# Kernel tuning notes

Measured on AMD Instinct MI355X. Metric: run time of the kernel, lower is better.

## Reference

```python
import jax, jax.numpy as jnp
import numpy as np
from jax import lax

BINS = 256
HSIG = 0.01
MS_WEIGHTS = np.array([0.0448, 0.2856, 0.3001, 0.2363, 0.1333], dtype=np.float32)


def _conv(x, w, b=None, pad='SAME', groups=1):
    out = lax.conv_general_dilated(x, w, (1, 1), pad,
                                   feature_group_count=groups,
                                   dimension_numbers=('NCHW', 'OIHW', 'NCHW'))
    if b is not None:
        out = out + b[None, :, None, None]
    return out


def _avg_pool(x, k):
    B, C, H, W = x.shape
    return x.reshape(B, C, H // k, k, W // k, k).mean(axis=(3, 5))


def _max_pool2(x):
    return lax.reduce_window(x, -jnp.inf, lax.max, (1, 1, 2, 2), (1, 1, 2, 2), 'VALID')


def _gauss_win():
    c = jnp.arange(11, dtype=jnp.float32) - 5.0
    g = jnp.exp(-(c * c) / (2.0 * 1.5 * 1.5))
    return g / g.sum()


def _gauss_filter(x, win):
    C = x.shape[1]
    wh = jnp.tile(win.reshape(1, 1, 11, 1), (C, 1, 1, 1))
    ww = jnp.tile(win.reshape(1, 1, 1, 11), (C, 1, 1, 1))
    x = _conv(x, wh, pad='VALID', groups=C)
    return _conv(x, ww, pad='VALID', groups=C)


def _ssim(X, Y, win):
    C1, C2 = 0.01 ** 2, 0.03 ** 2
    mu1 = _gauss_filter(X, win)
    mu2 = _gauss_filter(Y, win)
    s11 = _gauss_filter(X * X, win) - mu1 * mu1
    s22 = _gauss_filter(Y * Y, win) - mu2 * mu2
    s12 = _gauss_filter(X * Y, win) - mu1 * mu2
    cs = (2.0 * s12 + C2) / (s11 + s22 + C2)
    ssim = ((2.0 * mu1 * mu2 + C1) / (mu1 * mu1 + mu2 * mu2 + C1)) * cs
    return ssim.mean(axis=(2, 3)), cs.mean(axis=(2, 3))  # (B,C) each


def _ms_ssim(X, Y):
    win = _gauss_win()
    vals = []
    for i in range(5):
        s, c = _ssim(X, Y, win)
        vals.append(jax.nn.relu(s if i == 4 else c))
        if i < 4:
            X = _avg_pool(X, 2)
            Y = _avg_pool(Y, 2)
    v = jnp.stack(vals)  # (5,B,C)
    w = jnp.asarray(MS_WEIGHTS)[:, None, None]
    return jnp.prod(v ** w, axis=0).mean()


def _soft_hist(y, edges):
    # faithful to source: broadcast every pixel against 256 Gaussian bins,
    # sum over dim 0 (batch), then normalize to a distribution.
    h = jnp.exp(-0.5 * ((y[..., None] - edges) / HSIG) ** 2).sum(axis=0)  # (C,H,W,BINS)
    return h / h.sum()


def _vgg_feats(x, ws, bs):
    # VGG19 features[:16]: conv1_1..conv3_3, maxpool after conv idx 1 and 3.
    for i, (w, b) in enumerate(zip(ws, bs)):
        x = jax.nn.relu(_conv(x, w, b))
        if i in (1, 3):
            x = _max_pool2(x)
    return x


def combined_loss(y_true, y_pred, ws, bs):
    B, C, H, W = y_pred.shape
    diff = y_pred - y_true
    ad = jnp.abs(diff)
    # smooth L1 (beta=1)
    l1 = jnp.mean(jnp.where(ad < 1.0, 0.5 * diff * diff, ad - 0.5))
    # MS-SSIM loss
    msssim_l = 1.0 - _ms_ssim(y_true, y_pred)
    # VGG perceptual
    f1 = _vgg_feats(y_true, ws, bs)
    f2 = _vgg_feats(y_pred, ws, bs)
    perc = jnp.mean((f1 - f2) ** 2)
    # soft histogram
    edges = jnp.linspace(0.0, 1.0, BINS, dtype=jnp.float32)
    hist_l = jnp.mean(jnp.abs(_soft_hist(y_true, edges) - _soft_hist(y_pred, edges)))
    # PSNR loss: 40 - (-10*log10(mse))
    mse = jnp.mean(diff * diff)
    psnr_l = 40.0 + 10.0 * jnp.log10(mse)
    # color loss
    color_l = jnp.mean(jnp.abs(y_true.mean(axis=(1, 2, 3)) - y_pred.mean(axis=(1, 2, 3))))
    # exposure loss (16x16 avg pool of channel mean, target 0.6)
    exp_l = jnp.mean((_avg_pool(y_pred.mean(axis=1, keepdims=True), 16) - 0.6) ** 2)
    # illumination smoothness (counts faithful to source)
    hv = jnp.sum((y_pred[:, :, 1:, :] - y_pred[:, :, :-1, :]) ** 2)
    wv = jnp.sum((y_pred[:, :, :, 1:] - y_pred[:, :, :, :-1]) ** 2)
    ill = 2.0 * (hv / ((W - 1) * C) + wv / (W * (C - 1))) / B
    # spatial consistency: 4 neighbor-difference kernels on 4x4-pooled luminance
    K = jnp.array([[[0, 0, 0], [-1, 1, 0], [0, 0, 0]],
                   [[0, 0, 0], [0, 1, -1], [0, 0, 0]],
                   [[0, -1, 0], [0, 1, 0], [0, 0, 0]],
                   [[0, 0, 0], [0, 1, 0], [0, -1, 0]]], dtype=jnp.float32)[:, None]  # (4,1,3,3)
    op = _avg_pool(y_true.mean(axis=1, keepdims=True), 4)
    ep = _avg_pool(y_pred.mean(axis=1, keepdims=True), 4)
    spat = jnp.sum((_conv(op, K) - _conv(ep, K)) ** 2, axis=1, keepdims=True)  # (B,1,H/4,W/4)
    total = (1.0 * l1 + 0.06 * perc + 0.05 * hist_l + 0.0083 * psnr_l
             + 0.25 * color_l + 0.5 * msssim_l + 0.1 * exp_l + 0.1 * ill + 0.1 * spat)
    return jnp.mean(total)


def setup_inputs() -> dict:
    key = jax.random.key(0)
    ks = jax.random.split(key, 16)
    B, H, W = 2, 224, 224
    y_true = jax.random.uniform(ks[0], (B, 3, H, W), dtype=jnp.float32)
    y_pred = jax.random.uniform(ks[1], (B, 3, H, W), dtype=jnp.float32)
    chans = [(64, 3), (64, 64), (128, 64), (128, 128), (256, 128), (256, 256), (256, 256)]
    inp = {'y_true': y_true, 'y_pred': y_pred}
    for i, (co, ci) in enumerate(chans):
        std = float(np.sqrt(2.0 / (ci * 9)))
        inp[f'w{i}'] = jax.random.normal(ks[2 + i], (co, ci, 3, 3), dtype=jnp.float32) * std
        inp[f'b{i}'] = jnp.zeros((co,), dtype=jnp.float32)
    return inp


def reference(y_true, y_pred, w0, w1, w2, w3, w4, w5, w6, b0, b1, b2, b3, b4, b5, b6):
    ws = [w0, w1, w2, w3, w4, w5, w6]
    bs = [b0, b1, b2, b3, b4, b5, b6]
    return combined_loss(y_true, y_pred, ws, bs)
```

## Files before the change

kernel.cpp:

```cpp
#include <hip/hip_runtime.h>
#include <cmath>

typedef __attribute__((ext_vector_type(8))) short  short8;
typedef __attribute__((ext_vector_type(4))) float  floatx4;
typedef __attribute__((ext_vector_type(8))) unsigned short ushort8;
typedef __attribute__((ext_vector_type(8))) unsigned char uchar8v;

#define SLOT(i) ((i) * 16)
#define ACC_L1   0
#define ACC_MSE  1
#define ACC_ST0  2
#define ACC_ST1  3
#define ACC_SP0  4
#define ACC_SP1  5
#define ACC_HV   6
#define ACC_WV   7
#define ACC_EXP  8
#define ACC_SPAT 9
#define ACC_PERC 10
#define SSIM_SLOT(scale, cs, img) (256 + ((scale) * 12 + (cs) * 6 + (img)) * 16)

struct GW { float g[11]; };

__device__ __forceinline__ float waveSum(float v) {
#pragma unroll
  for (int o = 32; o > 0; o >>= 1) v += __shfl_down(v, o, 64);
  return v;
}

__device__ __forceinline__ float blockSum256(float v) {
  __shared__ float red[4];
  const int tid = threadIdx.x;
  v = waveSum(v);
  __syncthreads();
  if ((tid & 63) == 0) red[tid >> 6] = v;
  __syncthreads();
  return red[0] + red[1] + red[2] + red[3];
}

__device__ __forceinline__ unsigned int pk_fp8x4(float v0, float v1, float v2, float v3) {
  int p = __builtin_amdgcn_cvt_pk_fp8_f32(v0, v1, 0, false);
  p = __builtin_amdgcn_cvt_pk_fp8_f32(v2, v3, p, true);
  return (unsigned int)p;
}


struct PrepArgs {
  const float* w[6];
  int co[6], ci[6];
  int wcum[7];
  unsigned char* zp[6];
  int zH[6], zC[6];
  int zcum[7];
};

struct MegaArgs {
  PrepArgs pa;
  unsigned char* wdst;
  const float* w0;
  const float* b0;
  unsigned char* c1;
  float* pyrX;
  float* pyrY;
  float* acc;
  int nPrep, nBasic, nPyr, nPS;
};

__global__ __launch_bounds__(256) void mega_k(MegaArgs A,
                                              const float* __restrict__ yt,
                                              const float* __restrict__ yp) {
  __shared__ float smem[684];
  const int tid = threadIdx.x;
  int bid = blockIdx.x;

  if (bid < A.nPrep) {
    const int idx = bid * 256 + tid;
    const PrepArgs& a = A.pa;
    if (idx < a.wcum[6]) {
      int L = 0;
      while (idx >= a.wcum[L + 1]) ++L;
      const int r = idx - a.wcum[L];
      const int Cin = a.ci[L];
      const int cin = r % Cin;
      const int t = r / Cin;
      const int tap = t % 9;
      const int cout = t / 9;
      const float v = a.w[L][((size_t)cout * Cin + cin) * 9 + tap] * 8.0f;
      A.wdst[idx] = (unsigned char)(__builtin_amdgcn_cvt_pk_fp8_f32(v, v, 0, false) & 0xff);
      return;
    }
    const int zi = idx - a.wcum[6];
    if (zi >= a.zcum[6]) return;
    int b = 0;
    while (zi >= a.zcum[b + 1]) ++b;
    const int H = a.zH[b], C = a.zC[b];
    const int rowE = (H + 2) * C;
    const int per = 2 * rowE + 2 * H * C;
    int k = zi - a.zcum[b];
    const int pl = k / per;
    const int k0 = k - pl * per;
    size_t o;
    if (k0 < rowE) o = k0;
    else if (k0 < 2 * rowE) o = (size_t)(H + 1) * rowE + (k0 - rowE);
    else {
      const int kk = k0 - 2 * rowE;
      const int y = kk / (2 * C) + 1;
      const int r = kk % (2 * C);
      const int x = (r < C) ? 0 : (H + 1);
      const int c = (r < C) ? r : (r - C);
      o = (size_t)y * rowE + (size_t)x * C + c;
    }
    a.zp[b][(size_t)pl * (H + 2) * rowE + o] = 0;
    return;
  }
  bid -= A.nPrep;

  if (bid < A.nBasic) {
    float* acc = A.acc;
    const int i4 = bid * 256 + tid;
    const int idx = i4 * 4;
    const float4 t4 = *(const float4*)(yt + idx);
    const float4 p4 = *(const float4*)(yp + idx);
    float l1 = 0.f, mse = 0.f, st0 = 0.f, st1 = 0.f, sp0 = 0.f, sp1 = 0.f, hv = 0.f, wv = 0.f;
#define BTERM(tt, pp) { const float d = (pp) - (tt); const float ad = fabsf(d); \
                        l1 += (ad < 1.f) ? 0.5f * d * d : ad - 0.5f; mse += d * d; }
    BTERM(t4.x, p4.x) BTERM(t4.y, p4.y) BTERM(t4.z, p4.z) BTERM(t4.w, p4.w)
#undef BTERM
    const float ts = t4.x + t4.y + t4.z + t4.w;
    const float ps = p4.x + p4.y + p4.z + p4.w;
    if (i4 < 37632) { st0 = ts; sp0 = ps; } else { st1 = ts; sp1 = ps; }
    const int h = (idx / 224) % 224;
    if (h < 223) {
      const float4 pn = *(const float4*)(yp + idx + 224);
      float d;
      d = pn.x - p4.x; hv += d * d;
      d = pn.y - p4.y; hv += d * d;
      d = pn.z - p4.z; hv += d * d;
      d = pn.w - p4.w; hv += d * d;
    }
    {
      const int w = idx % 224;
      float d;
      d = p4.y - p4.x; wv += d * d;
      d = p4.z - p4.y; wv += d * d;
      d = p4.w - p4.z; wv += d * d;
      if (w < 220) { d = yp[idx + 4] - p4.w; wv += d * d; }
    }
    float s;
    s = blockSum256(l1);  if (tid == 0) atomicAdd(acc + SLOT(ACC_L1), s);
    s = blockSum256(mse); if (tid == 0) atomicAdd(acc + SLOT(ACC_MSE), s);
    s = blockSum256(st0); if (tid == 0) atomicAdd(acc + SLOT(ACC_ST0), s);
    s = blockSum256(st1); if (tid == 0) atomicAdd(acc + SLOT(ACC_ST1), s);
    s = blockSum256(sp0); if (tid == 0) atomicAdd(acc + SLOT(ACC_SP0), s);
    s = blockSum256(sp1); if (tid == 0) atomicAdd(acc + SLOT(ACC_SP1), s);
    s = blockSum256(hv);  if (tid == 0) atomicAdd(acc + SLOT(ACC_HV), s);
    s = blockSum256(wv);  if (tid == 0) atomicAdd(acc + SLOT(ACC_WV), s);
    return;
  }
  bid -= A.nBasic;

  if (bid < A.nPyr) {
    float (*sA)[17] = (float(*)[17])smem;
    float (*s1)[9]  = (float(*)[9])(smem + 272);
    float (*s2)[5]  = (float(*)[5])(smem + 344);
    float (*s3)[3]  = (float(*)[3])(smem + 364);
    const int tile = bid % 196;
    const int img = (bid / 196) % 6;
    const int zt = bid / (196 * 6);
    const int ty = tile / 14, tx = tile - ty * 14;
    const float* src = (zt ? yp : yt) + (size_t)img * 224 * 224;
    float* dst = zt ? A.pyrY : A.pyrX;
    const int r = tid >> 4, c = tid & 15;
    sA[r][c] = src[(size_t)(ty * 16 + r) * 224 + tx * 16 + c];
    __syncthreads();
    if (tid < 64) {
      const int r1 = tid >> 3, c1 = tid & 7;
      const float m = 0.25f * (sA[2 * r1][2 * c1] + sA[2 * r1][2 * c1 + 1] +
                               sA[2 * r1 + 1][2 * c1] + sA[2 * r1 + 1][2 * c1 + 1]);
      dst[(size_t)img * 12544 + (ty * 8 + r1) * 112 + tx * 8 + c1] = m;
      s1[r1][c1] = m;
    }
    __syncthreads();
    if (tid < 16) {
      const int r2 = tid >> 2, c2 = tid & 3;
      const float m = 0.25f * (s1[2 * r2][2 * c2] + s1[2 * r2][2 * c2 + 1] +
                               s1[2 * r2 + 1][2 * c2] + s1[2 * r2 + 1][2 * c2 + 1]);
      dst[75264 + (size_t)img * 3136 + (ty * 4 + r2) * 56 + tx * 4 + c2] = m;
      s2[r2][c2] = m;
    }
    __syncthreads();
    if (tid < 4) {
      const int r3 = tid >> 1, c3 = tid & 1;
      const float m = 0.25f * (s2[2 * r3][2 * c3] + s2[2 * r3][2 * c3 + 1] +
                               s2[2 * r3 + 1][2 * c3] + s2[2 * r3 + 1][2 * c3 + 1]);
      dst[94080 + (size_t)img * 784 + (ty * 2 + r3) * 28 + tx * 2 + c3] = m;
      s3[r3][c3] = m;
    }
    __syncthreads();
    if (tid == 0) {
      const float m = 0.25f * (s3[0][0] + s3[0][1] + s3[1][0] + s3[1][1]);
      dst[98784 + (size_t)img * 196 + ty * 14 + tx] = m;
    }
    return;
  }
  bid -= A.nPyr;

  if (bid < A.nPS) {
    float* acc = A.acc;
    float (*sOp)[19] = (float(*)[19])smem;
    float (*sEp)[19] = (float(*)[19])(smem + 342);
    const int b = bid >> 4;
    const int tq = bid & 15;
    const int ty0 = (tq >> 2) * 16, tx0 = (tq & 3) * 16;
    for (int e = tid; e < 18 * 18; e += 256) {
      const int r = e / 18, c = e - (e / 18) * 18;
      const int gy = ty0 - 1 + r, gx = tx0 - 1 + c;
      float vo = 0.f, ve = 0.f;
      if (gy >= 0 && gy < 56 && gx >= 0 && gx < 56) {
        float so = 0.f, se = 0.f;
        for (int ch = 0; ch < 3; ++ch)
#pragma unroll
          for (int dy = 0; dy < 4; ++dy) {
            const size_t off = (((size_t)b * 3 + ch) * 224 + (gy * 4 + dy)) * 224 + gx * 4;
            const float4 a = *(const float4*)(yt + off);
            const float4 ee = *(const float4*)(yp + off);
            so += a.x + a.y + a.z + a.w;
            se += ee.x + ee.y + ee.z + ee.w;
          }
        vo = so * (1.f / 48.f);
        ve = se * (1.f / 48.f);
      }
      sOp[r][c] = vo; sEp[r][c] = ve;
    }
    __syncthreads();
    float v = 0.f;
    {
      const int r = tid >> 4, c = tid & 15;
      const int gy = ty0 + r, gx = tx0 + c;
      if (gy < 56 && gx < 56) {
        const float oc = sOp[r + 1][c + 1], ec = sEp[r + 1][c + 1];
        const float ol = sOp[r + 1][c],     el = sEp[r + 1][c];
        const float orr = sOp[r + 1][c + 2], er = sEp[r + 1][c + 2];
        const float ou = sOp[r][c + 1],     eu = sEp[r][c + 1];
        const float od = sOp[r + 2][c + 1], ed = sEp[r + 2][c + 1];
        float d;
        d = (oc - ol) - (ec - el);   v += d * d;
        d = (oc - orr) - (ec - er);  v += d * d;
        d = (oc - ou) - (ec - eu);   v += d * d;
        d = (oc - od) - (ec - ed);   v += d * d;
      }
    }
    const float t = blockSum256(v);
    if (tid == 0) atomicAdd(acc + SLOT(ACC_SPAT), t);
    if (tid < 16) {
      const int ey = tid >> 2, ex = tid & 3;
      if (ty0 + 4 * ey < 56 && tx0 + 4 * ex < 56) {
        float ssum = 0.f;
#pragma unroll
        for (int dy = 0; dy < 4; ++dy)
#pragma unroll
          for (int dx = 0; dx < 4; ++dx)
            ssum += sEp[4 * ey + dy + 1][4 * ex + dx + 1];
        const float m = ssum * (1.f / 16.f) - 0.6f;
        atomicAdd(acc + SLOT(ACC_EXP), m * m);
      }
    }
    return;
  }
  bid -= A.nPS;

  {
    float (*sIn)[10][12] = (float(*)[10][12])smem;
    const int zf = bid / 784;
    const int rem = bid - zf * 784;
    const int by = rem / 28, bx = rem - by * 28;
    const int tx = tid & 7, ty = (tid >> 3) & 7, tz = tid >> 6;
    const int img = zf >> 1;
    const int zb = zf & 1;
    const float* in = ((img >> 1) ? yp : yt) + (size_t)(img & 1) * 3 * 224 * 224;
    const int x0 = bx << 3, y0 = by << 3;
    const int x = x0 + tx, y = y0 + ty;
    int wrow = (zb * 32 + tz * 8) * 27;
    wrow = __builtin_amdgcn_readfirstlane(wrow);

    for (int el = tid; el < 300; el += 256) {
      const int ci = el / 100;
      const int r2 = el - ci * 100;
      const int r = r2 / 10, cl = r2 - r * 10;
      const int gy = y0 - 1 + r, gx = x0 - 1 + cl;
      float v = 0.f;
      if (gy >= 0 && gy < 224 && gx >= 0 && gx < 224)
        v = in[((size_t)ci * 224 + gy) * 224 + gx];
      sIn[ci][r][cl] = v;
    }
    __syncthreads();

    float a[8];
#pragma unroll
    for (int j = 0; j < 8; ++j) a[j] = 0.f;
#pragma unroll
    for (int ci = 0; ci < 3; ++ci) {
      float xv[9];
#pragma unroll
      for (int ky = 0; ky < 3; ++ky)
#pragma unroll
        for (int kx = 0; kx < 3; ++kx)
          xv[ky * 3 + kx] = sIn[ci][ty + ky][tx + kx];
      const float* wp = A.w0 + wrow + ci * 9;
#pragma unroll
      for (int j = 0; j < 8; ++j)
#pragma unroll
        for (int k = 0; k < 9; ++k)
          a[j] = fmaf(xv[k], wp[27 * j + k], a[j]);
    }
    const int coB = zb * 32 + tz * 8;
    float r[8];
#pragma unroll
    for (int j = 0; j < 8; ++j) r[j] = fmaxf(a[j] + A.b0[coB + j], 0.f);
    const size_t o = (((size_t)(zb * 4 + img) * 226 + (y + 1)) * 226 + (x + 1)) * 32 + tz * 8;
    uint2 rv;
    rv.x = pk_fp8x4(r[0], r[1], r[2], r[3]);
    rv.y = pk_fp8x4(r[4], r[5], r[6], r[7]);
    *(uint2*)(A.c1 + o) = rv;
  }
}

__global__ __launch_bounds__(256) void ssim_all_k(const float* __restrict__ yt,
                                                  const float* __restrict__ yp,
                                                  const float* __restrict__ pyrX,
                                                  const float* __restrict__ pyrY,
                                                  float* __restrict__ acc, GW gw) {
  __shared__ float sX[26][27], sY[26][27];
  __shared__ float sV[5][16][27];
  const int bid = blockIdx.x;
  int s = 0;
  if (bid >= 196) s = 1;
  if (bid >= 245) s = 2;
  if (bid >= 254) s = 3;
  if (bid >= 258) s = 4;
  const int cumA[5]   = {0, 196, 245, 254, 258};
  const int tilesA[5] = {14, 7, 3, 2, 1};
  const int dimsA[5]  = {224, 112, 56, 28, 14};
  const int offsA[5]  = {0, 0, 75264, 94080, 98784};
  const int t = bid - cumA[s];
  const int tiles = tilesA[s];
  const int n = dimsA[s];
  const int m = n - 10;
  const int tid = threadIdx.x;
  const int img = blockIdx.y;
  const int ty0 = (t / tiles) * 16;
  const int tx0 = (t - (t / tiles) * tiles) * 16;
  const float* Xb = ((s == 0) ? yt : pyrX + offsA[s]) + (size_t)img * n * n;
  const float* Yb = ((s == 0) ? yp : pyrY + offsA[s]) + (size_t)img * n * n;

  for (int e = tid; e < 26 * 26; e += 256) {
    const int r = e / 26, c = e - (e / 26) * 26;
    const int gy = ty0 + r, gx = tx0 + c;
    float xv = 0.f, yv = 0.f;
    if (gy < n && gx < n) {
      xv = Xb[(size_t)gy * n + gx];
      yv = Yb[(size_t)gy * n + gx];
    }
    sX[r][c] = xv; sY[r][c] = yv;
  }
  __syncthreads();

  for (int e = tid; e < 16 * 26; e += 256) {
    const int r = e / 26, c = e - (e / 26) * 26;
    float sx = 0.f, sy = 0.f, sxx = 0.f, syy = 0.f, sxy = 0.f;
#pragma unroll
    for (int tt = 0; tt < 11; ++tt) {
      const float xv = sX[r + tt][c];
      const float yv = sY[r + tt][c];
      const float g = gw.g[tt];
      sx += g * xv; sy += g * yv;
      sxx += g * xv * xv; syy += g * yv * yv; sxy += g * xv * yv;
    }
    sV[0][r][c] = sx; sV[1][r][c] = sy;
    sV[2][r][c] = sxx; sV[3][r][c] = syy; sV[4][r][c] = sxy;
  }
  __syncthreads();

  float sv = 0.f, cv = 0.f;
  {
    const int r = tid >> 4, c = tid & 15;
    if (ty0 + r < m && tx0 + c < m) {
      float mu1 = 0.f, mu2 = 0.f, e11 = 0.f, e22 = 0.f, e12 = 0.f;
#pragma unroll
      for (int tt = 0; tt < 11; ++tt) {
        const float g = gw.g[tt];
        mu1 += g * sV[0][r][c + tt];
        mu2 += g * sV[1][r][c + tt];
        e11 += g * sV[2][r][c + tt];
        e22 += g * sV[3][r][c + tt];
        e12 += g * sV[4][r][c + tt];
      }
      const float C1 = 1e-4f, C2 = 9e-4f;
      const float s11 = e11 - mu1 * mu1;
      const float s22 = e22 - mu2 * mu2;
      const float s12 = e12 - mu1 * mu2;
      cv = (2.f * s12 + C2) / (s11 + s22 + C2);
      sv = ((2.f * mu1 * mu2 + C1) / (mu1 * mu1 + mu2 * mu2 + C1)) * cv;
    }
  }
  float tsum = blockSum256(sv);
  if (tid == 0) atomicAdd(acc + SSIM_SLOT(s, 0, img), tsum);
  tsum = blockSum256(cv);
  if (tid == 0) atomicAdd(acc + SSIM_SLOT(s, 1, img), tsum);
}

template<int CIN>
__global__ __launch_bounds__(256, 4) void conv_mfma(
    const unsigned char* __restrict__ in, const unsigned char* __restrict__ wtp,
    const float* __restrict__ bias, unsigned char* __restrict__ out,
    int W, int rowsPI) {
  constexpr int NSLAB = CIN / 32;
  constexpr int ASTB = 304;
  constexpr int BSTB = 48;
  constexpr int NBRUN = 6 * 66;
  constexpr int NACH = 32 * 18;
  constexpr int NBCH = NBRUN * 2;
  __shared__ unsigned char As[32 * ASTB];
  __shared__ unsigned char Bs[NBRUN * BSTB];

  const int tid = threadIdx.x;
  const int lane = tid & 63;
  const int wave = tid >> 6;
  const int quad = lane >> 4;
  const int lr = lane & 15;
  const int img = blockIdx.y / rowsPI;
  const int y0 = (blockIdx.y - img * rowsPI) * 4;
  const int x0 = blockIdx.x * 64;
  const int cob = blockIdx.z * 32;
  const int Wp = W + 2;
  const int H = rowsPI * 4;
  const size_t IPL = (size_t)(H + 2) * Wp * 32;
  const unsigned char* inI = in + (size_t)img * IPL;
  unsigned char* outI = out + ((size_t)blockIdx.z * 4 + img) * IPL;

  floatx4 acc[2][4];
#pragma unroll
  for (int m = 0; m < 2; ++m)
#pragma unroll
    for (int n = 0; n < 4; ++n) acc[m][n] = (floatx4){0.f, 0.f, 0.f, 0.f};

  const int abase = lr * ASTB + quad * 8;

  for (int s = 0; s < NSLAB; ++s) {
    __syncthreads();
#pragma unroll
    for (int i = 0; i < (NACH + 255) / 256; ++i) {
      const int ee = tid + i * 256;
      if (ee < NACH) {
        const int cout = ee / 18;
        const int rem = ee - cout * 18;
        const int tap = rem >> 1;
        const int part = rem & 1;
        const uint4 v = *(const uint4*)(wtp + ((size_t)(cob + cout) * 9 + tap) * CIN + s * 32 + part * 16);
        *(uint4*)(As + cout * ASTB + tap * 32 + part * 16) = v;
      }
    }
#pragma unroll
    for (int i = 0; i < (NBCH + 255) / 256; ++i) {
      const int ee = tid + i * 256;
      if (ee < NBCH) {
        const int part = ee & 1;
        const int run = ee >> 1;
        const int row = run / 66;
        const int px = run - row * 66;
        uint4 v = {0, 0, 0, 0};
        const int gx = x0 + px;
        if (gx < Wp)
          v = *(const uint4*)(inI + (size_t)s * 4 * IPL +
                              ((size_t)(y0 + row) * Wp + gx) * 32 + part * 16);
        *(uint4*)(Bs + run * BSTB + part * 16) = v;
      }
    }
    __syncthreads();

#pragma unroll
    for (int dy = 0; dy < 3; ++dy)
#pragma unroll
      for (int dx = 0; dx < 3; ++dx) {
        const int tap = dy * 3 + dx;
        const long af0 = *(const long*)(As + abase + tap * 32);
        const long af1 = *(const long*)(As + abase + 16 * ASTB + tap * 32);
        long bfr[4];
#pragma unroll
        for (int n = 0; n < 4; ++n)
          bfr[n] = *(const long*)(Bs + ((wave + dy) * 66 + n * 16 + lr + dx) * BSTB + quad * 8);
#pragma unroll
        for (int n = 0; n < 4; ++n) {
          acc[0][n] = __builtin_amdgcn_mfma_f32_16x16x32_fp8_fp8(af0, bfr[n], acc[0][n], 0, 0, 0);
          acc[1][n] = __builtin_amdgcn_mfma_f32_16x16x32_fp8_fp8(af1, bfr[n], acc[1][n], 0, 0, 0);
        }
      }
  }

#pragma unroll
  for (int m = 0; m < 2; ++m) {
    const int cb = cob + m * 16 + quad * 4;
#pragma unroll
    for (int n = 0; n < 4; ++n) {
      const int px = x0 + n * 16 + lr;
      if (px < W) {
        const float v0 = fmaxf(acc[m][n].x * 0.125f + bias[cb + 0], 0.f);
        const float v1 = fmaxf(acc[m][n].y * 0.125f + bias[cb + 1], 0.f);
        const float v2 = fmaxf(acc[m][n].z * 0.125f + bias[cb + 2], 0.f);
        const float v3 = fmaxf(acc[m][n].w * 0.125f + bias[cb + 3], 0.f);
        *(unsigned int*)(outI + ((size_t)(y0 + wave + 1) * Wp + px + 1) * 32 +
                         m * 16 + quad * 4) = pk_fp8x4(v0, v1, v2, v3);
      }
    }
  }
}

__global__ __launch_bounds__(256) void pool_nhwc(const unsigned char* __restrict__ in,
                                                 unsigned char* __restrict__ out,
                                                 int Ho, int Wo, int C) {
  const int per = Ho * Wo * (C / 8);
  const int idx = blockIdx.x * 256 + threadIdx.x;
  if (idx >= 4 * per) return;
  const int img = idx / per;
  const int k = idx - img * per;
  const int c8 = k % (C / 8);
  const int p = k / (C / 8);
  const int x = p % Wo, y = p / Wo;
  const int zb = c8 >> 2;
  const int cw = (c8 & 3) * 8;
  const int Wi = 2 * Wo + 2;
  const unsigned char* ib = in + ((size_t)(zb * 4 + img) * (2 * Ho + 2) * Wi +
                                  (size_t)(2 * y + 1) * Wi + (2 * x + 1)) * 32 + cw;
  const uchar8v a = *(const uchar8v*)(ib);
  const uchar8v b = *(const uchar8v*)(ib + 32);
  const uchar8v d = *(const uchar8v*)(ib + (size_t)Wi * 32);
  const uchar8v e = *(const uchar8v*)(ib + (size_t)Wi * 32 + 32);
  const uchar8v r = __builtin_elementwise_max(__builtin_elementwise_max(a, b),
                                              __builtin_elementwise_max(d, e));
  *(uchar8v*)(out + ((size_t)(zb * 4 + img) * (Ho + 2) * (Wo + 2) +
                     (size_t)(y + 1) * (Wo + 2) + (x + 1)) * 32 + cw) = r;
}

#define FP8D(av, bv, J) { const float dd = __builtin_amdgcn_cvt_f32_fp8((av), (J)) - \
                                           __builtin_amdgcn_cvt_f32_fp8((bv), (J)); \
                          v = fmaf(dd, dd, v); }
__global__ __launch_bounds__(256) void perc_k(const unsigned char* __restrict__ f,
                                              float* __restrict__ acc) {
  const int PER = 56 * 56 * 256 / 8;
  const size_t PL = (size_t)58 * 58 * 32;
  float v = 0.f;
  for (int ch = blockIdx.x * 256 + threadIdx.x; ch < 2 * PER; ch += 256 * 256) {
    const int q = ch / PER;
    const int r = ch - q * PER;
    const int e = r * 8;
    const int c = e & 255;
    const int p = e >> 8;
    const int x = p % 56, y = p / 56;
    const int zb = c >> 5;
    const int cw = c & 31;
    const size_t o = (size_t)(zb * 4 + q) * PL + ((size_t)(y + 1) * 58 + (x + 1)) * 32 + cw;
    const uint2 a = *(const uint2*)(f + o);
    const uint2 b = *(const uint2*)(f + o + 2 * PL);
    FP8D(a.x, b.x, 0) FP8D(a.x, b.x, 1) FP8D(a.x, b.x, 2) FP8D(a.x, b.x, 3)
    FP8D(a.y, b.y, 0) FP8D(a.y, b.y, 1) FP8D(a.y, b.y, 2) FP8D(a.y, b.y, 3)
  }
  const float t = blockSum256(v);
  if (threadIdx.x == 0) atomicAdd(acc + SLOT(ACC_PERC), t);
}

__global__ void final_k(const float* __restrict__ acc, float* __restrict__ out) {
  if (threadIdx.x != 0 || blockIdx.x != 0) return;
  const float NPIX = 2.f * 3.f * 224.f * 224.f;
  const float l1 = acc[SLOT(ACC_L1)] / NPIX;
  const float mse = acc[SLOT(ACC_MSE)] / NPIX;
  const float psnr = 40.f + 10.f * log10f(mse);
  const float cm = 1.f / (3.f * 224.f * 224.f);
  const float color = 0.5f * (fabsf(acc[SLOT(ACC_ST0)] - acc[SLOT(ACC_SP0)]) +
                              fabsf(acc[SLOT(ACC_ST1)] - acc[SLOT(ACC_SP1)])) * cm;
  const float ill = acc[SLOT(ACC_HV)] / 669.f + acc[SLOT(ACC_WV)] / 448.f;
  const float expl = acc[SLOT(ACC_EXP)] / 392.f;
  const float spat = acc[SLOT(ACC_SPAT)] / 6272.f;
  const float perc = acc[SLOT(ACC_PERC)] / 1605632.f;
  const float wms[5] = {0.0448f, 0.2856f, 0.3001f, 0.2363f, 0.1333f};
  const int ns[5] = {214, 102, 46, 18, 4};
  float msum = 0.f;
  for (int img = 0; img < 6; ++img) {
    float prod = 1.f;
    for (int s = 0; s < 5; ++s) {
      const float denom = (float)(ns[s] * ns[s]);
      float v = (s == 4) ? acc[SSIM_SLOT(s, 0, img)] / denom
                         : acc[SSIM_SLOT(s, 1, img)] / denom;
      v = fmaxf(v, 0.f);
      prod *= powf(v, wms[s]);
    }
    msum += prod;
  }
  const float msssim = msum / 6.f;
  out[0] = l1 + 0.06f * perc + 0.0083f * psnr + 0.25f * color +
           0.5f * (1.f - msssim) + 0.1f * expl + 0.1f * ill + 0.1f * spat;
}

extern "C" void kernel_launch(void* const* d_in, const int* in_sizes, int n_in,
                              void* d_out, int out_size, void* d_ws, size_t ws_size,
                              hipStream_t stream) {
  const float* yt = (const float*)d_in[0];
  const float* yp = (const float*)d_in[1];
  const float* W7[7]; const float* B7[7];
  for (int i = 0; i < 7; ++i) {
    W7[i] = (const float*)d_in[2 + 2 * i];
    B7[i] = (const float*)d_in[3 + 2 * i];
  }

  char* ws = (char*)d_ws;
  float* acc = (float*)ws;
  size_t off = 16384;
  auto align256 = [&]() { off = (off + 255) & ~(size_t)255; };
  align256(); unsigned char* C1  = (unsigned char*)(ws + off); off += (size_t)4 * 226 * 226 * 64;
  align256(); unsigned char* T0  = (unsigned char*)(ws + off); off += (size_t)4 * 226 * 226 * 64;
  align256(); unsigned char* Pl1 = (unsigned char*)(ws + off); off += (size_t)4 * 114 * 114 * 64;
  align256(); unsigned char* C3  = (unsigned char*)(ws + off); off += (size_t)4 * 114 * 114 * 128;
  align256(); unsigned char* Pl2 = (unsigned char*)(ws + off); off += (size_t)4 * 58 * 58 * 128;
  align256(); unsigned char* C5  = (unsigned char*)(ws + off); off += (size_t)4 * 58 * 58 * 256;
  align256(); unsigned char* C6  = (unsigned char*)(ws + off); off += (size_t)4 * 58 * 58 * 256;
  align256(); unsigned char* F   = (unsigned char*)(ws + off); off += (size_t)4 * 58 * 58 * 256;
  align256(); unsigned char* WT  = (unsigned char*)(ws + off); off += (size_t)1732608;
  align256(); float* pyrX = (float*)(ws + off); off += (size_t)100000 * 4;
  align256(); float* pyrY = (float*)(ws + off); off += (size_t)100000 * 4;
  if (ws_size < off) return;

  GW gw;
  {
    double vv[11]; double s = 0.0;
    for (int i = 0; i < 11; ++i) { const double c = i - 5.0; vv[i] = exp(-(c * c) / 4.5); s += vv[i]; }
    for (int i = 0; i < 11; ++i) gw.g[i] = (float)(vv[i] / s);
  }

  hipMemsetAsync(acc, 0, 16384, stream);

  const int co[7] = {64, 64, 128, 128, 256, 256, 256};
  const int ci[7] = {3, 64, 64, 128, 128, 256, 256};
  MegaArgs ma;
  size_t wtOff[7];
  {
    int e = 0;
    for (int i = 1; i < 7; ++i) {
      ma.pa.w[i - 1] = W7[i]; ma.pa.co[i - 1] = co[i]; ma.pa.ci[i - 1] = ci[i];
      ma.pa.wcum[i - 1] = e; wtOff[i] = (size_t)e; e += co[i] * 9 * ci[i];
    }
    ma.pa.wcum[6] = e;
    unsigned char* bufs[6] = {C1, Pl1, C3, Pl2, C5, C6};
    const int hh[6] = {224, 112, 112, 56, 56, 56};
    const int cc[6] = {64, 64, 128, 128, 256, 256};
    int z = 0;
    for (int i = 0; i < 6; ++i) {
      ma.pa.zp[i] = bufs[i]; ma.pa.zH[i] = hh[i]; ma.pa.zC[i] = 32;
      ma.pa.zcum[i] = z;
      z += (4 * cc[i] / 32) * (2 * (hh[i] + 2) * 32 + 2 * hh[i] * 32);
    }
    ma.pa.zcum[6] = z;
    ma.nPrep = (ma.pa.wcum[6] + z + 255) / 256;
  }
  ma.wdst = WT;
  ma.w0 = W7[0]; ma.b0 = B7[0];
  ma.c1 = C1;
  ma.pyrX = pyrX; ma.pyrY = pyrY;
  ma.acc = acc;
  ma.nBasic = 294;
  ma.nPyr = 196 * 6 * 2;
  ma.nPS = 32;
  const int nConv1 = 28 * 28 * 8;
  const int megaBlocks = ma.nPrep + ma.nBasic + ma.nPyr + ma.nPS + nConv1;

  mega_k<<<megaBlocks, 256, 0, stream>>>(ma, yt, yp);
  ssim_all_k<<<dim3(259, 6), 256, 0, stream>>>(yt, yp, pyrX, pyrY, acc, gw);

  conv_mfma<64> <<<dim3(4, 4 * 56, 2), 256, 0, stream>>>(C1,  WT + wtOff[1], B7[1], T0, 224, 56);
  pool_nhwc<<<(4 * 112 * 112 * 8 + 255) / 256, 256, 0, stream>>>(T0, Pl1, 112, 112, 64);
  conv_mfma<64> <<<dim3(2, 4 * 28, 4), 256, 0, stream>>>(Pl1, WT + wtOff[2], B7[2], C3, 112, 28);
  conv_mfma<128><<<dim3(2, 4 * 28, 4), 256, 0, stream>>>(C3,  WT + wtOff[3], B7[3], T0, 112, 28);
  pool_nhwc<<<(4 * 56 * 56 * 16 + 255) / 256, 256, 0, stream>>>(T0, Pl2, 56, 56, 128);
  conv_mfma<128><<<dim3(1, 4 * 14, 8), 256, 0, stream>>>(Pl2, WT + wtOff[4], B7[4], C5, 56, 14);
  conv_mfma<256><<<dim3(1, 4 * 14, 8), 256, 0, stream>>>(C5,  WT + wtOff[5], B7[5], C6, 56, 14);
  conv_mfma<256><<<dim3(1, 4 * 14, 8), 256, 0, stream>>>(C6,  WT + wtOff[6], B7[6], F,  56, 14);
  perc_k<<<256, 256, 0, stream>>>(F, acc);

  final_k<<<1, 64, 0, stream>>>(acc, (float*)d_out);
}
```

Before: 301.8 us.

## Move full-res SSIM into mega kernel, reorder blocks, vectorize weight prep and padding

Moves the scale-0 SSIM tiles, which read only the raw inputs, out of the separate SSIM kernel and into the mega kernel. The slower SSIM and conv1 blocks are scheduled first, and the follow-up kernel now handles only the pyramid scales. Weight fp8 conversion now writes 4 bytes per thread and border zeroing writes 16 bytes per thread, which cuts the number of prep blocks. The cost is larger shared memory per block in the mega kernel, which may lower occupancy for every branch.

```diff
diff --git a/kernel.cpp b/kernel.cpp
--- a/kernel.cpp
+++ b/kernel.cpp
@@ -50,7 +50,7 @@
   int co[6], ci[6];
   int wcum[7];
   unsigned char* zp[6];
-  int zH[6], zC[6];
+  int zH[6];
   int zcum[7];
 };
 
@@ -63,57 +63,187 @@
   float* pyrX;
   float* pyrY;
   float* acc;
-  int nPrep, nBasic, nPyr, nPS;
+  GW gw;
+  int nSsim0, nConv1, nPyr, nBasic, nPS, nPrep, nW4;
 };
 
 __global__ __launch_bounds__(256) void mega_k(MegaArgs A,
                                               const float* __restrict__ yt,
                                               const float* __restrict__ yp) {
-  __shared__ float smem[684];
+  __shared__ float smem[3564];
   const int tid = threadIdx.x;
   int bid = blockIdx.x;
 
-  if (bid < A.nPrep) {
-    const int idx = bid * 256 + tid;
-    const PrepArgs& a = A.pa;
-    if (idx < a.wcum[6]) {
-      int L = 0;
-      while (idx >= a.wcum[L + 1]) ++L;
-      const int r = idx - a.wcum[L];
-      const int Cin = a.ci[L];
-      const int cin = r % Cin;
-      const int t = r / Cin;
-      const int tap = t % 9;
-      const int cout = t / 9;
-      const float v = a.w[L][((size_t)cout * Cin + cin) * 9 + tap] * 8.0f;
-      A.wdst[idx] = (unsigned char)(__builtin_amdgcn_cvt_pk_fp8_f32(v, v, 0, false) & 0xff);
-      return;
-    }
-    const int zi = idx - a.wcum[6];
-    if (zi >= a.zcum[6]) return;
-    int b = 0;
-    while (zi >= a.zcum[b + 1]) ++b;
-    const int H = a.zH[b], C = a.zC[b];
-    const int rowE = (H + 2) * C;
-    const int per = 2 * rowE + 2 * H * C;
-    int k = zi - a.zcum[b];
-    const int pl = k / per;
-    const int k0 = k - pl * per;
-    size_t o;
-    if (k0 < rowE) o = k0;
-    else if (k0 < 2 * rowE) o = (size_t)(H + 1) * rowE + (k0 - rowE);
-    else {
-      const int kk = k0 - 2 * rowE;
-      const int y = kk / (2 * C) + 1;
-      const int r = kk % (2 * C);
-      const int x = (r < C) ? 0 : (H + 1);
-      const int c = (r < C) ? r : (r - C);
-      o = (size_t)y * rowE + (size_t)x * C + c;
-    }
-    a.zp[b][(size_t)pl * (H + 2) * rowE + o] = 0;
+  if (bid < A.nSsim0) {
+    float* acc = A.acc;
+    float (*sX)[27] = (float(*)[27])smem;
+    float (*sY)[27] = (float(*)[27])(smem + 702);
+    float (*sV)[16][27] = (float(*)[16][27])(smem + 1404);
+    const int img = bid / 196;
+    const int t = bid - img * 196;
+    const int n = 224, m = 214;
+    const int ty0 = (t / 14) * 16;
+    const int tx0 = (t - (t / 14) * 14) * 16;
+    const float* Xb = yt + (size_t)img * n * n;
+    const float* Yb = yp + (size_t)img * n * n;
+    for (int e = tid; e < 26 * 26; e += 256) {
+      const int r = e / 26, c = e - (e / 26) * 26;
+      const int gy = ty0 + r, gx = tx0 + c;
+      float xv = 0.f, yv = 0.f;
+      if (gy < n && gx < n) {
+        xv = Xb[(size_t)gy * n + gx];
+        yv = Yb[(size_t)gy * n + gx];
+      }
+      sX[r][c] = xv; sY[r][c] = yv;
+    }
+    __syncthreads();
+    for (int e = tid; e < 16 * 26; e += 256) {
+      const int r = e / 26, c = e - (e / 26) * 26;
+      float sx = 0.f, sy = 0.f, sxx = 0.f, syy = 0.f, sxy = 0.f;
+#pragma unroll
+      for (int tt = 0; tt < 11; ++tt) {
+        const float xv = sX[r + tt][c];
+        const float yv = sY[r + tt][c];
+        const float g = A.gw.g[tt];
+        sx += g * xv; sy += g * yv;
+        sxx += g * xv * xv; syy += g * yv * yv; sxy += g * xv * yv;
+      }
+      sV[0][r][c] = sx; sV[1][r][c] = sy;
+      sV[2][r][c] = sxx; sV[3][r][c] = syy; sV[4][r][c] = sxy;
+    }
+    __syncthreads();
+    float sv = 0.f, cv = 0.f;
+    {
+      const int r = tid >> 4, c = tid & 15;
+      if (ty0 + r < m && tx0 + c < m) {
+        float mu1 = 0.f, mu2 = 0.f, e11 = 0.f, e22 = 0.f, e12 = 0.f;
+#pragma unroll
+        for (int tt = 0; tt < 11; ++tt) {
+          const float g = A.gw.g[tt];
+          mu1 += g * sV[0][r][c + tt];
+          mu2 += g * sV[1][r][c + tt];
+          e11 += g * sV[2][r][c + tt];
+          e22 += g * sV[3][r][c + tt];
+          e12 += g * sV[4][r][c + tt];
+        }
+        const float C1 = 1e-4f, C2 = 9e-4f;
+        const float s11 = e11 - mu1 * mu1;
+        const float s22 = e22 - mu2 * mu2;
+        const float s12 = e12 - mu1 * mu2;
+        cv = (2.f * s12 + C2) / (s11 + s22 + C2);
+        sv = ((2.f * mu1 * mu2 + C1) / (mu1 * mu1 + mu2 * mu2 + C1)) * cv;
+      }
+    }
+    float tsum = blockSum256(sv);
+    if (tid == 0) atomicAdd(acc + SSIM_SLOT(0, 0, img), tsum);
+    tsum = blockSum256(cv);
+    if (tid == 0) atomicAdd(acc + SSIM_SLOT(0, 1, img), tsum);
     return;
   }
-  bid -= A.nPrep;
+  bid -= A.nSsim0;
+
+  if (bid < A.nConv1) {
+    float (*sIn)[10][12] = (float(*)[10][12])smem;
+    const int zf = bid / 784;
+    const int rem = bid - zf * 784;
+    const int by = rem / 28, bx = rem - by * 28;
+    const int tx = tid & 7, ty = (tid >> 3) & 7, tz = tid >> 6;
+    const int img = zf >> 1;
+    const int zb = zf & 1;
+    const float* in = ((img >> 1) ? yp : yt) + (size_t)(img & 1) * 3 * 224 * 224;
+    const int x0 = bx << 3, y0 = by << 3;
+    const int x = x0 + tx, y = y0 + ty;
+    int wrow = (zb * 32 + tz * 8) * 27;
+    wrow = __builtin_amdgcn_readfirstlane(wrow);
+
+    for (int el = tid; el < 300; el += 256) {
+      const int ci = el / 100;
+      const int r2 = el - ci * 100;
+      const int r = r2 / 10, cl = r2 - r * 10;
+      const int gy = y0 - 1 + r, gx = x0 - 1 + cl;
+      float v = 0.f;
+      if (gy >= 0 && gy < 224 && gx >= 0 && gx < 224)
+        v = in[((size_t)ci * 224 + gy) * 224 + gx];
+      sIn[ci][r][cl] = v;
+    }
+    __syncthreads();
+
+    float a[8];
+#pragma unroll
+    for (int j = 0; j < 8; ++j) a[j] = 0.f;
+#pragma unroll
+    for (int ci = 0; ci < 3; ++ci) {
+      float xv[9];
+#pragma unroll
+      for (int ky = 0; ky < 3; ++ky)
+#pragma unroll
+        for (int kx = 0; kx < 3; ++kx)
+          xv[ky * 3 + kx] = sIn[ci][ty + ky][tx + kx];
+      const float* wp = A.w0 + wrow + ci * 9;
+#pragma unroll
+      for (int j = 0; j < 8; ++j)
+#pragma unroll
+        for (int k = 0; k < 9; ++k)
+          a[j] = fmaf(xv[k], wp[27 * j + k], a[j]);
+    }
+    const int coB = zb * 32 + tz * 8;
+    float r[8];
+#pragma unroll
+    for (int j = 0; j < 8; ++j) r[j] = fmaxf(a[j] + A.b0[coB + j], 0.f);
+    const size_t o = (((size_t)(zb * 4 + img) * 226 + (y + 1)) * 226 + (x + 1)) * 32 + tz * 8;
+    uint2 rv;
+    rv.x = pk_fp8x4(r[0], r[1], r[2], r[3]);
+    rv.y = pk_fp8x4(r[4], r[5], r[6], r[7]);
+    *(uint2*)(A.c1 + o) = rv;
+    return;
+  }
+  bid -= A.nConv1;
+
+  if (bid < A.nPyr) {
+    float (*sA)[17] = (float(*)[17])smem;
+    float (*s1)[9]  = (float(*)[9])(smem + 272);
+    float (*s2)[5]  = (float(*)[5])(smem + 344);
+    float (*s3)[3]  = (float(*)[3])(smem + 364);
+    const int tile = bid % 196;
+    const int img = (bid / 196) % 6;
+    const int zt = bid / (196 * 6);
+    const int ty = tile / 14, tx = tile - ty * 14;
+    const float* src = (zt ? yp : yt) + (size_t)img * 224 * 224;
+    float* dst = zt ? A.pyrY : A.pyrX;
+    const int r = tid >> 4, c = tid & 15;
+    sA[r][c] = src[(size_t)(ty * 16 + r) * 224 + tx * 16 + c];
+    __syncthreads();
+    if (tid < 64) {
+      const int r1 = tid >> 3, c1 = tid & 7;
+      const float m = 0.25f * (sA[2 * r1][2 * c1] + sA[2 * r1][2 * c1 + 1] +
+                               sA[2 * r1 + 1][2 * c1] + sA[2 * r1 + 1][2 * c1 + 1]);
+      dst[(size_t)img * 12544 + (ty * 8 + r1) * 112 + tx * 8 + c1] = m;
+      s1[r1][c1] = m;
+    }
+    __syncthreads();
+    if (tid < 16) {
+      const int r2 = tid >> 2, c2 = tid & 3;
+      const float m = 0.25f * (s1[2 * r2][2 * c2] + s1[2 * r2][2 * c2 + 1] +
+                               s1[2 * r2 + 1][2 * c2] + s1[2 * r2 + 1][2 * c2 + 1]);
+      dst[75264 + (size_t)img * 3136 + (ty * 4 + r2) * 56 + tx * 4 + c2] = m;
+      s2[r2][c2] = m;
+    }
+    __syncthreads();
+    if (tid < 4) {
+      const int r3 = tid >> 1, c3 = tid & 1;
+      const float m = 0.25f * (s2[2 * r3][2 * c3] + s2[2 * r3][2 * c3 + 1] +
+                               s2[2 * r3 + 1][2 * c3] + s2[2 * r3 + 1][2 * c3 + 1]);
+      dst[94080 + (size_t)img * 784 + (ty * 2 + r3) * 28 + tx * 2 + c3] = m;
+      s3[r3][c3] = m;
+    }
+    __syncthreads();
+    if (tid == 0) {
+      const float m = 0.25f * (s3[0][0] + s3[0][1] + s3[1][0] + s3[1][1]);
+      dst[98784 + (size_t)img * 196 + ty * 14 + tx] = m;
+    }
+    return;
+  }
+  bid -= A.nPyr;
 
   if (bid < A.nBasic) {
     float* acc = A.acc;
@@ -159,52 +289,6 @@
   }
   bid -= A.nBasic;
 
-  if (bid < A.nPyr) {
-    float (*sA)[17] = (float(*)[17])smem;
-    float (*s1)[9]  = (float(*)[9])(smem + 272);
-    float (*s2)[5]  = (float(*)[5])(smem + 344);
-    float (*s3)[3]  = (float(*)[3])(smem + 364);
-    const int tile = bid % 196;
-    const int img = (bid / 196) % 6;
-    const int zt = bid / (196 * 6);
-    const int ty = tile / 14, tx = tile - ty * 14;
-    const float* src = (zt ? yp : yt) + (size_t)img * 224 * 224;
-    float* dst = zt ? A.pyrY : A.pyrX;
-    const int r = tid >> 4, c = tid & 15;
-    sA[r][c] = src[(size_t)(ty * 16 + r) * 224 + tx * 16 + c];
-    __syncthreads();
-    if (tid < 64) {
-      const int r1 = tid >> 3, c1 = tid & 7;
-      const float m = 0.25f * (sA[2 * r1][2 * c1] + sA[2 * r1][2 * c1 + 1] +
-                               sA[2 * r1 + 1][2 * c1] + sA[2 * r1 + 1][2 * c1 + 1]);
-      dst[(size_t)img * 12544 + (ty * 8 + r1) * 112 + tx * 8 + c1] = m;
-      s1[r1][c1] = m;
-    }
-    __syncthreads();
-    if (tid < 16) {
-      const int r2 = tid >> 2, c2 = tid & 3;
-      const float m = 0.25f * (s1[2 * r2][2 * c2] + s1[2 * r2][2 * c2 + 1] +
-                               s1[2 * r2 + 1][2 * c2] + s1[2 * r2 + 1][2 * c2 + 1]);
-      dst[75264 + (size_t)img * 3136 + (ty * 4 + r2) * 56 + tx * 4 + c2] = m;
-      s2[r2][c2] = m;
-    }
-    __syncthreads();
-    if (tid < 4) {
-      const int r3 = tid >> 1, c3 = tid & 1;
-      const float m = 0.25f * (s2[2 * r3][2 * c3] + s2[2 * r3][2 * c3 + 1] +
-                               s2[2 * r3 + 1][2 * c3] + s2[2 * r3 + 1][2 * c3 + 1]);
-      dst[94080 + (size_t)img * 784 + (ty * 2 + r3) * 28 + tx * 2 + c3] = m;
-      s3[r3][c3] = m;
-    }
-    __syncthreads();
-    if (tid == 0) {
-      const float m = 0.25f * (s3[0][0] + s3[0][1] + s3[1][0] + s3[1][1]);
-      dst[98784 + (size_t)img * 196 + ty * 14 + tx] = m;
-    }
-    return;
-  }
-  bid -= A.nPyr;
-
   if (bid < A.nPS) {
     float* acc = A.acc;
     float (*sOp)[19] = (float(*)[19])smem;
@@ -270,77 +354,59 @@
   bid -= A.nPS;
 
   {
-    float (*sIn)[10][12] = (float(*)[10][12])smem;
-    const int zf = bid / 784;
-    const int rem = bid - zf * 784;
-    const int by = rem / 28, bx = rem - by * 28;
-    const int tx = tid & 7, ty = (tid >> 3) & 7, tz = tid >> 6;
-    const int img = zf >> 1;
-    const int zb = zf & 1;
-    const float* in = ((img >> 1) ? yp : yt) + (size_t)(img & 1) * 3 * 224 * 224;
-    const int x0 = bx << 3, y0 = by << 3;
-    const int x = x0 + tx, y = y0 + ty;
-    int wrow = (zb * 32 + tz * 8) * 27;
-    wrow = __builtin_amdgcn_readfirstlane(wrow);
-
-    for (int el = tid; el < 300; el += 256) {
-      const int ci = el / 100;
-      const int r2 = el - ci * 100;
-      const int r = r2 / 10, cl = r2 - r * 10;
-      const int gy = y0 - 1 + r, gx = x0 - 1 + cl;
-      float v = 0.f;
-      if (gy >= 0 && gy < 224 && gx >= 0 && gx < 224)
-        v = in[((size_t)ci * 224 + gy) * 224 + gx];
-      sIn[ci][r][cl] = v;
-    }
-    __syncthreads();
-
-    float a[8];
-#pragma unroll
-    for (int j = 0; j < 8; ++j) a[j] = 0.f;
-#pragma unroll
-    for (int ci = 0; ci < 3; ++ci) {
-      float xv[9];
-#pragma unroll
-      for (int ky = 0; ky < 3; ++ky)
-#pragma unroll
-        for (int kx = 0; kx < 3; ++kx)
-          xv[ky * 3 + kx] = sIn[ci][ty + ky][tx + kx];
-      const float* wp = A.w0 + wrow + ci * 9;
-#pragma unroll
-      for (int j = 0; j < 8; ++j)
-#pragma unroll
-        for (int k = 0; k < 9; ++k)
-          a[j] = fmaf(xv[k], wp[27 * j + k], a[j]);
-    }
-    const int coB = zb * 32 + tz * 8;
-    float r[8];
-#pragma unroll
-    for (int j = 0; j < 8; ++j) r[j] = fmaxf(a[j] + A.b0[coB + j], 0.f);
-    const size_t o = (((size_t)(zb * 4 + img) * 226 + (y + 1)) * 226 + (x + 1)) * 32 + tz * 8;
-    uint2 rv;
-    rv.x = pk_fp8x4(r[0], r[1], r[2], r[3]);
-    rv.y = pk_fp8x4(r[4], r[5], r[6], r[7]);
-    *(uint2*)(A.c1 + o) = rv;
-  }
-}
-
-__global__ __launch_bounds__(256) void ssim_all_k(const float* __restrict__ yt,
-                                                  const float* __restrict__ yp,
-                                                  const float* __restrict__ pyrX,
-                                                  const float* __restrict__ pyrY,
-                                                  float* __restrict__ acc, GW gw) {
+    const int idx = bid * 256 + tid;
+    const PrepArgs& a = A.pa;
+    if (idx < A.nW4) {
+      const int e0 = idx * 4;
+      int L = 0;
+      while (e0 >= a.wcum[L + 1]) ++L;
+      const int r = e0 - a.wcum[L];
+      const int Cin = a.ci[L];
+      const int cin = r % Cin;
+      const int t = r / Cin;
+      const int tap = t % 9;
+      const int cout = t / 9;
+      const float* wsrc = a.w[L] + ((size_t)cout * Cin + cin) * 9 + tap;
+      *(unsigned int*)(A.wdst + e0) =
+          pk_fp8x4(wsrc[0] * 8.f, wsrc[9] * 8.f, wsrc[18] * 8.f, wsrc[27] * 8.f);
+      return;
+    }
+    const int zi = idx - A.nW4;
+    if (zi >= a.zcum[6]) return;
+    int b = 0;
+    while (zi >= a.zcum[b + 1]) ++b;
+    const int H = a.zH[b];
+    const int rowE = (H + 2) * 32;
+    const int perC = (2 * rowE + 2 * H * 32) >> 4;
+    const int k = zi - a.zcum[b];
+    const int pl = k / perC;
+    const int k0 = (k - pl * perC) << 4;
+    size_t o;
+    if (k0 < rowE) o = k0;
+    else if (k0 < 2 * rowE) o = (size_t)(H + 1) * rowE + (k0 - rowE);
+    else {
+      const int kk = k0 - 2 * rowE;
+      const int y = kk / 64 + 1;
+      const int r = kk & 63;
+      o = (size_t)y * rowE + ((r < 32) ? (size_t)r : ((size_t)(H + 1) * 32 + (r - 32)));
+    }
+    *(uint4*)(a.zp[b] + (size_t)pl * (H + 2) * rowE + o) = (uint4){0, 0, 0, 0};
+  }
+}
+
+__global__ __launch_bounds__(256) void ssim_rest_k(const float* __restrict__ pyrX,
+                                                   const float* __restrict__ pyrY,
+                                                   float* __restrict__ acc, GW gw) {
   __shared__ float sX[26][27], sY[26][27];
   __shared__ float sV[5][16][27];
   const int bid = blockIdx.x;
-  int s = 0;
-  if (bid >= 196) s = 1;
-  if (bid >= 245) s = 2;
-  if (bid >= 254) s = 3;
-  if (bid >= 258) s = 4;
-  const int cumA[5]   = {0, 196, 245, 254, 258};
-  const int tilesA[5] = {14, 7, 3, 2, 1};
-  const int dimsA[5]  = {224, 112, 56, 28, 14};
+  int s = 1;
+  if (bid >= 49) s = 2;
+  if (bid >= 58) s = 3;
+  if (bid >= 62) s = 4;
+  const int cumA[5]   = {0, 0, 49, 58, 62};
+  const int tilesA[5] = {0, 7, 3, 2, 1};
+  const int dimsA[5]  = {0, 112, 56, 28, 14};
   const int offsA[5]  = {0, 0, 75264, 94080, 98784};
   const int t = bid - cumA[s];
   const int tiles = tilesA[s];
@@ -350,8 +416,8 @@
   const int img = blockIdx.y;
   const int ty0 = (t / tiles) * 16;
   const int tx0 = (t - (t / tiles) * tiles) * 16;
-  const float* Xb = ((s == 0) ? yt : pyrX + offsA[s]) + (size_t)img * n * n;
-  const float* Yb = ((s == 0) ? yp : pyrY + offsA[s]) + (size_t)img * n * n;
+  const float* Xb = pyrX + offsA[s] + (size_t)img * n * n;
+  const float* Yb = pyrY + offsA[s] + (size_t)img * n * n;
 
   for (int e = tid; e < 26 * 26; e += 256) {
     const int r = e / 26, c = e - (e / 26) * 26;
@@ -648,31 +714,35 @@
       ma.pa.wcum[i - 1] = e; wtOff[i] = (size_t)e; e += co[i] * 9 * ci[i];
     }
     ma.pa.wcum[6] = e;
+    ma.nW4 = e / 4;
     unsigned char* bufs[6] = {C1, Pl1, C3, Pl2, C5, C6};
     const int hh[6] = {224, 112, 112, 56, 56, 56};
     const int cc[6] = {64, 64, 128, 128, 256, 256};
     int z = 0;
     for (int i = 0; i < 6; ++i) {
-      ma.pa.zp[i] = bufs[i]; ma.pa.zH[i] = hh[i]; ma.pa.zC[i] = 32;
+      ma.pa.zp[i] = bufs[i]; ma.pa.zH[i] = hh[i];
       ma.pa.zcum[i] = z;
-      z += (4 * cc[i] / 32) * (2 * (hh[i] + 2) * 32 + 2 * hh[i] * 32);
+      const int perC = (2 * (hh[i] + 2) * 32 + 2 * hh[i] * 32) >> 4;
+      z += (4 * cc[i] / 32) * perC;
     }
     ma.pa.zcum[6] = z;
-    ma.nPrep = (ma.pa.wcum[6] + z + 255) / 256;
+    ma.nPrep = (ma.nW4 + z + 255) / 256;
   }
   ma.wdst = WT;
   ma.w0 = W7[0]; ma.b0 = B7[0];
   ma.c1 = C1;
   ma.pyrX = pyrX; ma.pyrY = pyrY;
   ma.acc = acc;
+  ma.gw = gw;
+  ma.nSsim0 = 196 * 6;
+  ma.nConv1 = 28 * 28 * 8;
+  ma.nPyr = 196 * 6 * 2;
   ma.nBasic = 294;
-  ma.nPyr = 196 * 6 * 2;
   ma.nPS = 32;
-  const int nConv1 = 28 * 28 * 8;
-  const int megaBlocks = ma.nPrep + ma.nBasic + ma.nPyr + ma.nPS + nConv1;
+  const int megaBlocks = ma.nSsim0 + ma.nConv1 + ma.nPyr + ma.nBasic + ma.nPS + ma.nPrep;
 
   mega_k<<<megaBlocks, 256, 0, stream>>>(ma, yt, yp);
-  ssim_all_k<<<dim3(259, 6), 256, 0, stream>>>(yt, yp, pyrX, pyrY, acc, gw);
+  ssim_rest_k<<<dim3(63, 6), 256, 0, stream>>>(pyrX, pyrY, acc, gw);
 
   conv_mfma<64> <<<dim3(4, 4 * 56, 2), 256, 0, stream>>>(C1,  WT + wtOff[1], B7[1], T0, 224, 56);
   pool_nhwc<<<(4 * 112 * 112 * 8 + 255) / 256, 256, 0, stream>>>(T0, Pl1, 112, 112, 64);
```

Result: slower. 320.7 us (+6.2%).
